# Performance work log

Measured on AMD Instinct MI355X. Metric: run time of the kernel, lower is better.

## Reference

```python
import jax, jax.numpy as jnp
import numpy as np

N = 100000   # nodes
E = 1000000  # edges
IN = 64      # in_dim
H = 4        # hidden heads
D = 32       # num_hidden (per-head dim)
C = 32       # num_classes
NEG_SLOPE = 0.2


def setup_inputs() -> dict:
    key = jax.random.key(0)
    ks = jax.random.split(key, 9)
    def init(k, shape, fan):
        return jax.random.normal(k, shape, jnp.float32) * np.float32(1.0 / np.sqrt(fan))
    return {
        "T": jax.random.normal(ks[0], (N, IN), jnp.float32),
        "src": jax.random.randint(ks[1], (E,), 0, N),
        "dst": jax.random.randint(ks[2], (E,), 0, N),
        "W0": init(ks[3], (IN, H * D), IN),
        "al0": init(ks[4], (H, D), D),
        "ar0": init(ks[5], (H, D), D),
        "W1": init(ks[6], (H * D, C), H * D),
        "al1": init(ks[7], (1, C), C),
        "ar1": init(ks[8], (1, C), C),
    }


def _gat_layer(x, W, al, ar, src, dst, heads, dim):
    # DGL GATConv: linear proj -> per-edge additive attention -> edge softmax
    # (segment softmax over incoming edges of each dst node) -> weighted sum.
    h = (x @ W).reshape(N, heads, dim)                      # [N,H,D]
    el = (h * al[None]).sum(-1)                             # [N,H]
    er = (h * ar[None]).sum(-1)                             # [N,H]
    e = jax.nn.leaky_relu(el[src] + er[dst], NEG_SLOPE)     # [E,H]
    m = jax.ops.segment_max(e, dst, num_segments=N)         # [N,H]
    ex = jnp.exp(e - m[dst])                                # [E,H]
    ssum = jax.ops.segment_sum(ex, dst, num_segments=N)     # [N,H]
    alpha = ex / ssum[dst]                                  # [E,H]
    msg = h[src] * alpha[:, :, None]                        # [E,H,D]
    return jax.ops.segment_sum(msg, dst, num_segments=N)    # [N,H,D]


def reference(T, src, dst, W0, al0, ar0, W1, al1, ar1):
    # hidden GAT layer: concat heads + elu
    h = _gat_layer(T, W0, al0, ar0, src, dst, H, D)
    h = jax.nn.elu(h).reshape(N, H * D)
    # output GAT layer: 1 head, mean over heads, no activation
    out = _gat_layer(h, W1, al1, ar1, src, dst, 1, C).mean(axis=1)  # [N,C]
    # AvgPooling over the single graph -> [1,C]
    return out.mean(axis=0, keepdims=True)
```

## Files before the change

### kernel.cpp

```cpp
#include <hip/hip_runtime.h>
#include <math.h>

#define NN 100000
#define NE 1000000
#define CAP 32
#define BSH 8
#define BNODES 256
#define NBUK 391
#define BUKCAP 6144
#define EPB 4096
#define ABLK 245

constexpr size_t AL(size_t x){ return (x + 255) & ~size_t(255); }
constexpr size_t OFF_H0  = 0;
constexpr size_t OFF_H1P = OFF_H0  + AL(size_t(NN)*32*4);
constexpr size_t OFF_EL0 = OFF_H1P + AL(size_t(NN)*16*4);
constexpr size_t OFF_ER0 = OFF_EL0 + AL(size_t(NN)*4*4);
constexpr size_t OFF_EL1 = OFF_ER0 + AL(size_t(NN)*4*4);
constexpr size_t OFF_ER1 = OFF_EL1 + AL(size_t(NN)*4);
constexpr size_t OFF_CNT = OFF_ER1 + AL(size_t(NN)*4);
constexpr size_t OFF_CSRF= OFF_CNT + AL(size_t(NN)*4);
constexpr size_t OFF_BUK = OFF_CSRF+ AL(size_t(NN)*CAP*4);
constexpr size_t OFF_BUKC= OFF_BUK + AL(size_t(NBUK)*BUKCAP*4);
constexpr size_t OFF_P2  = OFF_BUKC+ AL(size_t(NBUK)*4);
constexpr size_t OFF_PART= OFF_P2  + AL(25*32*4);

using f32x2 = __attribute__((ext_vector_type(2))) float;

__device__ __forceinline__ float lrelu(float x){ return x >= 0.f ? x : 0.2f*x; }
__device__ __forceinline__ unsigned f2bf(float x){
  unsigned b = __float_as_uint(x);
  return (b + 0x7FFFu + ((b >> 16) & 1u)) >> 16;
}
__device__ __forceinline__ float bflo(unsigned u){ return __uint_as_float(u << 16); }
__device__ __forceinline__ float bfhi(unsigned u){ return __uint_as_float(u & 0xFFFF0000u); }

__device__ __forceinline__ void fp8fma(uint2 u, float x, float* acc){
  f32x2 a0 = __builtin_amdgcn_cvt_pk_f32_fp8((int)u.x, false);
  f32x2 a1 = __builtin_amdgcn_cvt_pk_f32_fp8((int)u.x, true);
  f32x2 a2 = __builtin_amdgcn_cvt_pk_f32_fp8((int)u.y, false);
  f32x2 a3 = __builtin_amdgcn_cvt_pk_f32_fp8((int)u.y, true);
  acc[0] = fmaf(x, a0.x, acc[0]); acc[1] = fmaf(x, a0.y, acc[1]);
  acc[2] = fmaf(x, a1.x, acc[2]); acc[3] = fmaf(x, a1.y, acc[3]);
  acc[4] = fmaf(x, a2.x, acc[4]); acc[5] = fmaf(x, a2.y, acc[5]);
  acc[6] = fmaf(x, a3.x, acc[6]); acc[7] = fmaf(x, a3.y, acc[7]);
}

__global__ __launch_bounds__(256) void k_gemm1(const float* __restrict__ T,
    const float* __restrict__ W0, const float* __restrict__ al0, const float* __restrict__ ar0,
    unsigned* __restrict__ h0p, float* __restrict__ el0, float* __restrict__ er0,
    int* __restrict__ bukCnt){
  __shared__ float w[64*128];
  __shared__ float tr[64][65];
  int t = threadIdx.x;
  int base = blockIdx.x * 64;
  if (blockIdx.x == 0){
    for (int i = t; i < NBUK; i += 256) bukCnt[i] = 0;
  }
  {
    const float4* W4 = (const float4*)W0;
    float4* w4 = (float4*)w;
    #pragma unroll
    for (int i = 0; i < 8; ++i) w4[t + 256*i] = W4[t + 256*i];
  }
  for (int i = t; i < 1024; i += 256){
    int rr = i >> 4, f = i & 15;
    int n = base + rr;
    float4 v = make_float4(0.f,0.f,0.f,0.f);
    if (n < NN) v = ((const float4*)(T + (size_t)n*64))[f];
    int kc = f << 2;
    tr[rr][kc] = v.x; tr[rr][kc+1] = v.y; tr[rr][kc+2] = v.z; tr[rr][kc+3] = v.w;
  }
  __syncthreads();
  int tx = t & 15, ty = t >> 4;
  int r0 = ty * 4;
  int jA = tx * 4, jB = 64 + tx * 4;
  float accA[4][4], accB[4][4];
  #pragma unroll
  for (int rr = 0; rr < 4; ++rr)
    #pragma unroll
    for (int j = 0; j < 4; ++j){ accA[rr][j] = 0.f; accB[rr][j] = 0.f; }
  #pragma unroll 2
  for (int k = 0; k < 64; ++k){
    float4 wA = *(const float4*)&w[k*128 + jA];
    float4 wB = *(const float4*)&w[k*128 + jB];
    #pragma unroll
    for (int rr = 0; rr < 4; ++rr){
      float a = tr[r0 + rr][k];
      accA[rr][0] = fmaf(a, wA.x, accA[rr][0]);
      accA[rr][1] = fmaf(a, wA.y, accA[rr][1]);
      accA[rr][2] = fmaf(a, wA.z, accA[rr][2]);
      accA[rr][3] = fmaf(a, wA.w, accA[rr][3]);
      accB[rr][0] = fmaf(a, wB.x, accB[rr][0]);
      accB[rr][1] = fmaf(a, wB.y, accB[rr][1]);
      accB[rr][2] = fmaf(a, wB.z, accB[rr][2]);
      accB[rr][3] = fmaf(a, wB.w, accB[rr][3]);
    }
  }
  float alA[4], arA[4], alB[4], arB[4];
  #pragma unroll
  for (int j = 0; j < 4; ++j){
    alA[j] = al0[jA+j]; arA[j] = ar0[jA+j];
    alB[j] = al0[jB+j]; arB[j] = ar0[jB+j];
  }
  #pragma unroll
  for (int rr = 0; rr < 4; ++rr){
    int n = base + r0 + rr;
    float vlA=0.f, vrA=0.f, vlB=0.f, vrB=0.f;
    #pragma unroll
    for (int j = 0; j < 4; ++j){
      vlA = fmaf(accA[rr][j], alA[j], vlA);
      vrA = fmaf(accA[rr][j], arA[j], vrA);
      vlB = fmaf(accB[rr][j], alB[j], vlB);
      vrB = fmaf(accB[rr][j], arB[j], vrB);
    }
    int pa = __builtin_amdgcn_cvt_pk_fp8_f32(accA[rr][0], accA[rr][1], 0, false);
    pa     = __builtin_amdgcn_cvt_pk_fp8_f32(accA[rr][2], accA[rr][3], pa, true);
    int pb = __builtin_amdgcn_cvt_pk_fp8_f32(accB[rr][0], accB[rr][1], 0, false);
    pb     = __builtin_amdgcn_cvt_pk_fp8_f32(accB[rr][2], accB[rr][3], pb, true);
    #pragma unroll
    for (int m = 1; m <= 4; m <<= 1){
      vlA += __shfl_xor(vlA, m); vrA += __shfl_xor(vrA, m);
      vlB += __shfl_xor(vlB, m); vrB += __shfl_xor(vrB, m);
    }
    if (n < NN){
      h0p[(size_t)n*32 + tx]      = (unsigned)pa;
      h0p[(size_t)n*32 + 16 + tx] = (unsigned)pb;
      if (tx == 0){
        el0[n*4 + 0] = vlA; er0[n*4 + 0] = vrA;
        el0[n*4 + 2] = vlB; er0[n*4 + 2] = vrB;
      } else if (tx == 8){
        el0[n*4 + 1] = vlA; er0[n*4 + 1] = vrA;
        el0[n*4 + 3] = vlB; er0[n*4 + 3] = vrB;
      }
    }
  }
}

__global__ __launch_bounds__(256) void k_bucket(const int* __restrict__ src,
    const int* __restrict__ dst, int* __restrict__ bukCnt, unsigned* __restrict__ buk){
  __shared__ int hist[NBUK];
  __shared__ int base[NBUK];
  int t = threadIdx.x;
  int e0 = blockIdx.x * EPB;
  int ecnt = min(EPB, NE - e0);
  int myd[16], mys[16];
  for (int i = t; i < NBUK; i += 256) hist[i] = 0;
  __syncthreads();
  #pragma unroll
  for (int q = 0; q < 16; ++q){
    int i = t + q*256;
    if (i < ecnt){
      myd[q] = dst[e0 + i];
      mys[q] = src[e0 + i];
      atomicAdd(&hist[myd[q] >> BSH], 1);
    }
  }
  __syncthreads();
  for (int i = t; i < NBUK; i += 256){
    int c = hist[i];
    base[i] = c ? atomicAdd(&bukCnt[i], (c + 15) & ~15) : 0;
  }
  __syncthreads();
  for (int i = t; i < NBUK; i += 256) hist[i] = 0;
  __syncthreads();
  #pragma unroll
  for (int q = 0; q < 16; ++q){
    int i = t + q*256;
    if (i < ecnt){
      int b = myd[q] >> BSH;
      int pos = base[b] + atomicAdd(&hist[b], 1);
      if (pos < BUKCAP)
        buk[(size_t)b * BUKCAP + pos] = ((unsigned)mys[q] << BSH) | (unsigned)(myd[q] & (BNODES-1));
    }
  }
  __syncthreads();
  for (int i = t; i < NBUK; i += 256){
    int c = hist[i];
    if (c){
      int p0 = base[i] + c;
      int p1 = base[i] + ((c + 15) & ~15);
      for (int p = p0; p < p1; ++p)
        if (p < BUKCAP) buk[(size_t)i * BUKCAP + p] = 0xFFFFFFFFu;
    }
  }
}

__global__ __launch_bounds__(256) void k_csr(const unsigned* __restrict__ buk,
    const int* __restrict__ bukCnt, int* __restrict__ cnt, int* __restrict__ csrF){
  __shared__ int lcnt[BNODES];
  __shared__ int lcsr[BNODES*CAP];
  int t = threadIdx.x;
  int b = blockIdx.x;
  int nbase = b << BSH;
  for (int i = t; i < BNODES; i += 256) lcnt[i] = 0;
  __syncthreads();
  int ecnt = min(bukCnt[b], BUKCAP);
  for (int i = t; i < ecnt; i += 256){
    unsigned v = buk[(size_t)b * BUKCAP + i];
    if (v == 0xFFFFFFFFu) continue;
    int dloc = v & (BNODES-1);
    int slot = atomicAdd(&lcnt[dloc], 1);
    if (slot < CAP) lcsr[(dloc << 5) + slot] = (int)(v >> BSH);
  }
  __syncthreads();
  for (int i = t; i < BNODES; i += 256){
    int n = nbase + i;
    if (n < NN) cnt[n] = min(lcnt[i], CAP);
  }
  const int4* l4 = (const int4*)lcsr;
  int4* g4 = (int4*)csrF;
  for (int k = t; k < BNODES*(CAP/4); k += 256){
    int nloc = k >> 3, q = k & 7;
    int n = nbase + nloc;
    if (n < NN && q*4 < lcnt[nloc]) g4[((size_t)n << 3) + q] = l4[k];
  }
}

__global__ __launch_bounds__(256) void k_agg0g2(const unsigned* __restrict__ h0p,
    const float* __restrict__ el0, const float* __restrict__ er0,
    const int* __restrict__ cnt, const int* __restrict__ csrF,
    const float* __restrict__ W1, const float* __restrict__ al1, const float* __restrict__ ar1,
    unsigned* __restrict__ h1pg, float* __restrict__ el1, float* __restrict__ er1){
  __shared__ int   idxs[4][4][33];
  __shared__ float exv [4][4][33][4];
  __shared__ float wl[128*32];
  __shared__ unsigned hrowU[16][68];
  int t = threadIdx.x;
  {
    const float4* W4 = (const float4*)W1;
    float4* w4 = (float4*)wl;
    #pragma unroll
    for (int i = 0; i < 4; ++i) w4[t + 256*i] = W4[t + 256*i];
  }
  int wib = t >> 6, lane = t & 63;
  int g = lane >> 4, l4 = lane & 15;
  int n = blockIdx.x*16 + wib*4 + g;
  int deg = min(cnt[n], CAP);
  const float4* el4p = (const float4*)el0;
  float4 er4 = ((const float4*)er0)[n];
  for (int e = l4; e < deg; e += 16){
    int sj = csrF[(n << 5) + e];
    float4 e4 = el4p[sj];
    float4 x;
    x.x = __expf(lrelu(e4.x + er4.x));
    x.y = __expf(lrelu(e4.y + er4.y));
    x.z = __expf(lrelu(e4.z + er4.z));
    x.w = __expf(lrelu(e4.w + er4.w));
    idxs[wib][g][e] = sj;
    *(float4*)&exv[wib][g][e][0] = x;
  }
  __builtin_amdgcn_wave_barrier();
  int head = l4 >> 2;
  float acc[8];
  #pragma unroll
  for (int i = 0; i < 8; ++i) acc[i] = 0.f;
  float ssum = 0.f;
  int j = 0;
  for (; j + 3 < deg; j += 4){
    int s0 = idxs[wib][g][j],   s1 = idxs[wib][g][j+1];
    int s2 = idxs[wib][g][j+2], s3 = idxs[wib][g][j+3];
    float x0 = exv[wib][g][j][head],   x1 = exv[wib][g][j+1][head];
    float x2 = exv[wib][g][j+2][head], x3 = exv[wib][g][j+3][head];
    uint2 u0 = *(const uint2*)&h0p[(size_t)s0*32 + l4*2];
    uint2 u1 = *(const uint2*)&h0p[(size_t)s1*32 + l4*2];
    uint2 u2 = *(const uint2*)&h0p[(size_t)s2*32 + l4*2];
    uint2 u3 = *(const uint2*)&h0p[(size_t)s3*32 + l4*2];
    fp8fma(u0, x0, acc); fp8fma(u1, x1, acc);
    fp8fma(u2, x2, acc); fp8fma(u3, x3, acc);
    ssum += x0 + x1 + x2 + x3;
  }
  for (; j < deg; ++j){
    int sa = idxs[wib][g][j];
    float xa = exv[wib][g][j][head];
    uint2 ua = *(const uint2*)&h0p[(size_t)sa*32 + l4*2];
    fp8fma(ua, xa, acc);
    ssum += xa;
  }
  float inv = (deg > 0) ? 1.f / ssum : 0.f;
  float o[8];
  #pragma unroll
  for (int i = 0; i < 8; ++i){
    float v = acc[i] * inv;
    o[i] = v > 0.f ? v : expm1f(v);
  }
  uint4 up;
  up.x = (f2bf(o[1]) << 16) | f2bf(o[0]);
  up.y = (f2bf(o[3]) << 16) | f2bf(o[2]);
  up.z = (f2bf(o[5]) << 16) | f2bf(o[4]);
  up.w = (f2bf(o[7]) << 16) | f2bf(o[6]);
  int nb = wib*4 + g;
  *(uint4*)&hrowU[nb][l4*4] = up;
  __syncthreads();
  int r = t >> 4, cc = t & 15;
  float ac0 = 0.f, ac1 = 0.f;
  #pragma unroll 8
  for (int f = 0; f < 64; ++f){
    unsigned hu = hrowU[r][f];
    float a0 = bflo(hu), a1 = bfhi(hu);
    float2 w0 = *(const float2*)&wl[(2*f)*32   + 2*cc];
    float2 w1 = *(const float2*)&wl[(2*f+1)*32 + 2*cc];
    ac0 = fmaf(a0, w0.x, ac0); ac0 = fmaf(a1, w1.x, ac0);
    ac1 = fmaf(a0, w0.y, ac1); ac1 = fmaf(a1, w1.y, ac1);
  }
  int nOut = blockIdx.x*16 + r;
  float vl = ac0*al1[2*cc] + ac1*al1[2*cc+1];
  float vr = ac0*ar1[2*cc] + ac1*ar1[2*cc+1];
  #pragma unroll
  for (int m = 1; m <= 8; m <<= 1){
    vl += __shfl_xor(vl, m); vr += __shfl_xor(vr, m);
  }
  h1pg[(size_t)nOut*16 + cc] = (f2bf(ac1) << 16) | f2bf(ac0);
  if (cc == 0){ el1[nOut] = vl; er1[nOut] = vr; }
}

__global__ __launch_bounds__(256) void k_agg1(const unsigned* __restrict__ h1pg,
    const float* __restrict__ el1, const float* __restrict__ er1,
    const int* __restrict__ cnt, const int* __restrict__ csrF, float* __restrict__ part){
  __shared__ int   idxs[4][4][33];
  __shared__ float exs [4][4][33];
  __shared__ float sp[4][32];
  int t = threadIdx.x;
  int wib = t >> 6, lane = t & 63;
  int g = lane >> 4, l4 = lane & 15;
  int n = blockIdx.x*16 + wib*4 + g;
  int deg = min(cnt[n], CAP);
  float ern = er1[n];
  for (int e = l4; e < deg; e += 16){
    int sj = csrF[(n << 5) + e];
    idxs[wib][g][e] = sj;
    exs[wib][g][e] = __expf(lrelu(el1[sj] + ern));
  }
  __builtin_amdgcn_wave_barrier();
  float a0 = 0.f, a1 = 0.f, ssum = 0.f;
  int j = 0;
  for (; j + 3 < deg; j += 4){
    int s0 = idxs[wib][g][j],   s1 = idxs[wib][g][j+1];
    int s2 = idxs[wib][g][j+2], s3 = idxs[wib][g][j+3];
    float x0 = exs[wib][g][j],   x1 = exs[wib][g][j+1];
    float x2 = exs[wib][g][j+2], x3 = exs[wib][g][j+3];
    unsigned u0 = h1pg[(size_t)s0*16 + l4];
    unsigned u1 = h1pg[(size_t)s1*16 + l4];
    unsigned u2 = h1pg[(size_t)s2*16 + l4];
    unsigned u3 = h1pg[(size_t)s3*16 + l4];
    a0 = fmaf(x0, bflo(u0), a0); a1 = fmaf(x0, bfhi(u0), a1);
    a0 = fmaf(x1, bflo(u1), a0); a1 = fmaf(x1, bfhi(u1), a1);
    a0 = fmaf(x2, bflo(u2), a0); a1 = fmaf(x2, bfhi(u2), a1);
    a0 = fmaf(x3, bflo(u3), a0); a1 = fmaf(x3, bfhi(u3), a1);
    ssum += x0 + x1 + x2 + x3;
  }
  for (; j < deg; ++j){
    int sa = idxs[wib][g][j];
    float xa = exs[wib][g][j];
    unsigned ua = h1pg[(size_t)sa*16 + l4];
    a0 = fmaf(xa, bflo(ua), a0); a1 = fmaf(xa, bfhi(ua), a1);
    ssum += xa;
  }
  float inv = (deg > 0) ? 1.f / ssum : 0.f;
  a0 *= inv; a1 *= inv;
  a0 += __shfl_xor(a0, 16); a0 += __shfl_xor(a0, 32);
  a1 += __shfl_xor(a1, 16); a1 += __shfl_xor(a1, 32);
  if (lane < 16){ sp[wib][2*l4] = a0; sp[wib][2*l4+1] = a1; }
  __syncthreads();
  if (t < 32){
    part[(size_t)blockIdx.x*32 + t] = sp[0][t] + sp[1][t] + sp[2][t] + sp[3][t];
  }
}

__global__ __launch_bounds__(256) void k_red(const float* __restrict__ part, float* __restrict__ part2){
  __shared__ float red[8][32];
  int t = threadIdx.x;
  int c = t & 31, g = t >> 5;
  size_t base = (size_t)blockIdx.x * 250;
  float s = 0.f;
  for (int r = g; r < 250; r += 8) s += part[(base + r)*32 + c];
  red[g][c] = s;
  __syncthreads();
  if (t < 32){
    float tot = 0.f;
    #pragma unroll
    for (int g2 = 0; g2 < 8; ++g2) tot += red[g2][t];
    part2[(size_t)blockIdx.x*32 + t] = tot;
  }
}

__global__ void k_final(const float* __restrict__ part2, float* __restrict__ out){
  int c = threadIdx.x;
  if (c < 32){
    float s = 0.f;
    #pragma unroll
    for (int r = 0; r < 25; ++r) s += part2[r*32 + c];
    out[c] = s * (1.f / NN);
  }
}

extern "C" void kernel_launch(void* const* d_in, const int* in_sizes, int n_in,
                              void* d_out, int out_size, void* d_ws, size_t ws_size,
                              hipStream_t stream) {
  (void)in_sizes; (void)n_in; (void)out_size; (void)ws_size;
  const float* T   = (const float*)d_in[0];
  const int*  srcI = (const int*)d_in[1];
  const int*  dstI = (const int*)d_in[2];
  const float* W0  = (const float*)d_in[3];
  const float* al0 = (const float*)d_in[4];
  const float* ar0 = (const float*)d_in[5];
  const float* W1  = (const float*)d_in[6];
  const float* al1 = (const float*)d_in[7];
  const float* ar1 = (const float*)d_in[8];

  char* ws = (char*)d_ws;
  unsigned* h0p  = (unsigned*)(ws + OFF_H0);
  unsigned* h1pg = (unsigned*)(ws + OFF_H1P);
  float* el0  = (float*)(ws + OFF_EL0);
  float* er0  = (float*)(ws + OFF_ER0);
  float* el1  = (float*)(ws + OFF_EL1);
  float* er1  = (float*)(ws + OFF_ER1);
  int*   cnt  = (int*)(ws + OFF_CNT);
  int*   csrF = (int*)(ws + OFF_CSRF);
  unsigned* buk = (unsigned*)(ws + OFF_BUK);
  int*   bukCnt = (int*)(ws + OFF_BUKC);
  float* part2 = (float*)(ws + OFF_P2);
  float* part = (float*)(ws + OFF_PART);
  float* out  = (float*)d_out;

  const int NB_G  = 1563;
  const int NB_A  = NN / 16;

  k_gemm1  <<<NB_G, 256, 0, stream>>>(T, W0, al0, ar0, h0p, el0, er0, bukCnt);
  k_bucket <<<ABLK, 256, 0, stream>>>(srcI, dstI, bukCnt, buk);
  k_csr    <<<NBUK, 256, 0, stream>>>(buk, bukCnt, cnt, csrF);
  k_agg0g2 <<<NB_A, 256, 0, stream>>>(h0p, el0, er0, cnt, csrF,
                                      W1, al1, ar1, h1pg, el1, er1);
  k_agg1   <<<NB_A, 256, 0, stream>>>(h1pg, el1, er1, cnt, csrF, part);
  k_red    <<<25, 256, 0, stream>>>(part, part2);
  k_final  <<<1, 64, 0, stream>>>(part2, out);
}
```

Baseline: 147.6 us.

## Store layer-1 features as FP8 and read W1 directly from global

Layer-1 projected features are now packed as FP8 (e4m3) pairs instead of bf16, halving the bytes gathered per edge in the second aggregation kernel. The gather decodes with hardware FP8 conversion and selects the needed half per lane. Separately, the 16 KB LDS staging of W1 in the fused aggregation kernel is removed and weights are read from global/L1, which cuts LDS use and per-block copy cost. FP8 storage loses precision, which may hurt tolerance, and the direct global weight reads may cost more than the LDS reads did.

```diff
diff --git a/kernel.cpp b/kernel.cpp
--- a/kernel.cpp
+++ b/kernel.cpp
@@ -14,7 +14,7 @@
 constexpr size_t AL(size_t x){ return (x + 255) & ~size_t(255); }
 constexpr size_t OFF_H0  = 0;
 constexpr size_t OFF_H1P = OFF_H0  + AL(size_t(NN)*32*4);
-constexpr size_t OFF_EL0 = OFF_H1P + AL(size_t(NN)*16*4);
+constexpr size_t OFF_EL0 = OFF_H1P + AL(size_t(NN)*8*4);
 constexpr size_t OFF_ER0 = OFF_EL0 + AL(size_t(NN)*4*4);
 constexpr size_t OFF_EL1 = OFF_ER0 + AL(size_t(NN)*4*4);
 constexpr size_t OFF_ER1 = OFF_EL1 + AL(size_t(NN)*4);
@@ -221,18 +221,11 @@
     const float* __restrict__ el0, const float* __restrict__ er0,
     const int* __restrict__ cnt, const int* __restrict__ csrF,
     const float* __restrict__ W1, const float* __restrict__ al1, const float* __restrict__ ar1,
-    unsigned* __restrict__ h1pg, float* __restrict__ el1, float* __restrict__ er1){
+    unsigned* __restrict__ h1f, float* __restrict__ el1, float* __restrict__ er1){
   __shared__ int   idxs[4][4][33];
   __shared__ float exv [4][4][33][4];
-  __shared__ float wl[128*32];
   __shared__ unsigned hrowU[16][68];
   int t = threadIdx.x;
-  {
-    const float4* W4 = (const float4*)W1;
-    float4* w4 = (float4*)wl;
-    #pragma unroll
-    for (int i = 0; i < 4; ++i) w4[t + 256*i] = W4[t + 256*i];
-  }
   int wib = t >> 6, lane = t & 63;
   int g = lane >> 4, l4 = lane & 15;
   int n = blockIdx.x*16 + wib*4 + g;
@@ -298,8 +291,8 @@
   for (int f = 0; f < 64; ++f){
     unsigned hu = hrowU[r][f];
     float a0 = bflo(hu), a1 = bfhi(hu);
-    float2 w0 = *(const float2*)&wl[(2*f)*32   + 2*cc];
-    float2 w1 = *(const float2*)&wl[(2*f+1)*32 + 2*cc];
+    float2 w0 = *(const float2*)&W1[(2*f)*32   + 2*cc];
+    float2 w1 = *(const float2*)&W1[(2*f+1)*32 + 2*cc];
     ac0 = fmaf(a0, w0.x, ac0); ac0 = fmaf(a1, w1.x, ac0);
     ac1 = fmaf(a0, w0.y, ac1); ac1 = fmaf(a1, w1.y, ac1);
   }
@@ -310,11 +303,14 @@
   for (int m = 1; m <= 8; m <<= 1){
     vl += __shfl_xor(vl, m); vr += __shfl_xor(vr, m);
   }
-  h1pg[(size_t)nOut*16 + cc] = (f2bf(ac1) << 16) | f2bf(ac0);
+  int pk = __builtin_amdgcn_cvt_pk_fp8_f32(ac0, ac1, 0, false) & 0xFFFF;
+  int pr = __shfl_xor(pk, 1);
+  if ((cc & 1) == 0)
+    h1f[(size_t)nOut*8 + (cc >> 1)] = (unsigned)(pk | (pr << 16));
   if (cc == 0){ el1[nOut] = vl; er1[nOut] = vr; }
 }
 
-__global__ __launch_bounds__(256) void k_agg1(const unsigned* __restrict__ h1pg,
+__global__ __launch_bounds__(256) void k_agg1(const unsigned* __restrict__ h1f,
     const float* __restrict__ el1, const float* __restrict__ er1,
     const int* __restrict__ cnt, const int* __restrict__ csrF, float* __restrict__ part){
   __shared__ int   idxs[4][4][33];
@@ -332,6 +328,8 @@
     exs[wib][g][e] = __expf(lrelu(el1[sj] + ern));
   }
   __builtin_amdgcn_wave_barrier();
+  int word = l4 >> 1;
+  bool hiSel = (l4 & 1);
   float a0 = 0.f, a1 = 0.f, ssum = 0.f;
   int j = 0;
   for (; j + 3 < deg; j += 4){
@@ -339,21 +337,37 @@
     int s2 = idxs[wib][g][j+2], s3 = idxs[wib][g][j+3];
     float x0 = exs[wib][g][j],   x1 = exs[wib][g][j+1];
     float x2 = exs[wib][g][j+2], x3 = exs[wib][g][j+3];
-    unsigned u0 = h1pg[(size_t)s0*16 + l4];
-    unsigned u1 = h1pg[(size_t)s1*16 + l4];
-    unsigned u2 = h1pg[(size_t)s2*16 + l4];
-    unsigned u3 = h1pg[(size_t)s3*16 + l4];
-    a0 = fmaf(x0, bflo(u0), a0); a1 = fmaf(x0, bfhi(u0), a1);
-    a0 = fmaf(x1, bflo(u1), a0); a1 = fmaf(x1, bfhi(u1), a1);
-    a0 = fmaf(x2, bflo(u2), a0); a1 = fmaf(x2, bfhi(u2), a1);
-    a0 = fmaf(x3, bflo(u3), a0); a1 = fmaf(x3, bfhi(u3), a1);
+    unsigned u0 = h1f[(size_t)s0*8 + word];
+    unsigned u1 = h1f[(size_t)s1*8 + word];
+    unsigned u2 = h1f[(size_t)s2*8 + word];
+    unsigned u3 = h1f[(size_t)s3*8 + word];
+    f32x2 lo, hi, p;
+    lo = __builtin_amdgcn_cvt_pk_f32_fp8((int)u0, false);
+    hi = __builtin_amdgcn_cvt_pk_f32_fp8((int)u0, true);
+    p.x = hiSel ? hi.x : lo.x; p.y = hiSel ? hi.y : lo.y;
+    a0 = fmaf(x0, p.x, a0); a1 = fmaf(x0, p.y, a1);
+    lo = __builtin_amdgcn_cvt_pk_f32_fp8((int)u1, false);
+    hi = __builtin_amdgcn_cvt_pk_f32_fp8((int)u1, true);
+    p.x = hiSel ? hi.x : lo.x; p.y = hiSel ? hi.y : lo.y;
+    a0 = fmaf(x1, p.x, a0); a1 = fmaf(x1, p.y, a1);
+    lo = __builtin_amdgcn_cvt_pk_f32_fp8((int)u2, false);
+    hi = __builtin_amdgcn_cvt_pk_f32_fp8((int)u2, true);
+    p.x = hiSel ? hi.x : lo.x; p.y = hiSel ? hi.y : lo.y;
+    a0 = fmaf(x2, p.x, a0); a1 = fmaf(x2, p.y, a1);
+    lo = __builtin_amdgcn_cvt_pk_f32_fp8((int)u3, false);
+    hi = __builtin_amdgcn_cvt_pk_f32_fp8((int)u3, true);
+    p.x = hiSel ? hi.x : lo.x; p.y = hiSel ? hi.y : lo.y;
+    a0 = fmaf(x3, p.x, a0); a1 = fmaf(x3, p.y, a1);
     ssum += x0 + x1 + x2 + x3;
   }
   for (; j < deg; ++j){
     int sa = idxs[wib][g][j];
     float xa = exs[wib][g][j];
-    unsigned ua = h1pg[(size_t)sa*16 + l4];
-    a0 = fmaf(xa, bflo(ua), a0); a1 = fmaf(xa, bfhi(ua), a1);
+    unsigned ua = h1f[(size_t)sa*8 + word];
+    f32x2 lo = __builtin_amdgcn_cvt_pk_f32_fp8((int)ua, false);
+    f32x2 hi = __builtin_amdgcn_cvt_pk_f32_fp8((int)ua, true);
+    float px = hiSel ? hi.x : lo.x, py = hiSel ? hi.y : lo.y;
+    a0 = fmaf(xa, px, a0); a1 = fmaf(xa, py, a1);
     ssum += xa;
   }
   float inv = (deg > 0) ? 1.f / ssum : 0.f;
@@ -410,7 +424,7 @@
 
   char* ws = (char*)d_ws;
   unsigned* h0p  = (unsigned*)(ws + OFF_H0);
-  unsigned* h1pg = (unsigned*)(ws + OFF_H1P);
+  unsigned* h1f  = (unsigned*)(ws + OFF_H1P);
   float* el0  = (float*)(ws + OFF_EL0);
   float* er0  = (float*)(ws + OFF_ER0);
   float* el1  = (float*)(ws + OFF_EL1);
@@ -430,8 +444,8 @@
   k_bucket <<<ABLK, 256, 0, stream>>>(srcI, dstI, bukCnt, buk);
   k_csr    <<<NBUK, 256, 0, stream>>>(buk, bukCnt, cnt, csrF);
   k_agg0g2 <<<NB_A, 256, 0, stream>>>(h0p, el0, er0, cnt, csrF,
-                                      W1, al1, ar1, h1pg, el1, er1);
-  k_agg1   <<<NB_A, 256, 0, stream>>>(h1pg, el1, er1, cnt, csrF, part);
+                                      W1, al1, ar1, h1f, el1, er1);
+  k_agg1   <<<NB_A, 256, 0, stream>>>(h1f, el1, er1, cnt, csrF, part);
   k_red    <<<25, 256, 0, stream>>>(part, part2);
   k_final  <<<1, 64, 0, stream>>>(part2, out);
 }
```

New measurement: 201.6 us. 36.6% more time.
